# Kernel tuning notes

Hardware: AMD Instinct MI355X
Metric: run time of the kernel (lower is better)

## Reference

```python
import jax, jax.numpy as jnp
import numpy as np

NUM_CLASSES = 17
NUM_ENSEMBLE = 10
TAU = 10.0
TOP_K = 20  # min(self.k=20, filter_K=200)
EPS = 1e-12


def _l2norm(x, axis=-1):
    # matches F.normalize: x / max(||x||, 1e-12)
    n = jnp.sqrt(jnp.sum(x * x, axis=axis, keepdims=True))
    return x / jnp.maximum(n, EPS)


def _batch_ensemble(x, weight, alpha_be, gamma_be, ensemble_bias):
    # x: [M, D1] -> [E, M, D2]  (BatchEnsemble.forward, kept in [E, M, D2] layout)
    r = x[None, :, :] * alpha_be[:, None, :]              # [E, M, D1]
    w = jnp.einsum('emd,od->emo', r, weight)              # [E, M, D2]
    return w * gamma_be[:, None, :] + ensemble_bias[:, None, :]


def _compute_logits(z, supports, labels, weight, alpha_be, gamma_be, ensemble_bias):
    mlp_z = _batch_ensemble(z, weight, alpha_be, gamma_be, ensemble_bias)         # [E, B, D2]
    mlp_s = _batch_ensemble(supports, weight, alpha_be, gamma_be, ensemble_bias)  # [E, N, D2]
    lbl = labels / (jnp.sum(labels, axis=0, keepdims=True) + EPS)                 # [N, C]
    centroids = jnp.einsum('nc,end->ecd', lbl, mlp_s)                             # [E, C, D2]
    zn = _l2norm(mlp_z)
    cn = _l2norm(centroids)
    return TAU * jnp.einsum('ebd,ecd->ebc', zn, cn)                               # [E, B, C]


def _cosine_distance(X, Y):
    Xn = _l2norm(X, axis=1)
    Yn = _l2norm(Y, axis=1)
    XX = jnp.sum(Xn * Xn, axis=1)[:, None]   # [B, 1]
    YY = jnp.sum(Yn * Yn, axis=1)            # [N]
    XY = 2.0 * (Xn @ Yn.T)                   # [B, N]
    return XX + YY - XY


def _target_generation(z, supports, labels, weight, alpha_be, gamma_be, ensemble_bias):
    dist = _cosine_distance(z, supports)      # [B, N]
    W = jnp.exp(-dist)
    B = W.shape[0]
    _, idx = jax.lax.top_k(W, TOP_K)                                   # [B, K]
    mask = jnp.zeros_like(W).at[jnp.arange(B)[:, None], idx].set(1.0)  # [B, N]
    temp = _compute_logits(supports, supports, labels, weight, alpha_be, gamma_be, ensemble_bias)  # [E, N, C]
    tgt_oh = jax.nn.one_hot(jnp.argmax(temp, axis=-1), NUM_CLASSES, dtype=temp.dtype)  # [E, N, C]
    soft = jax.nn.softmax(temp, axis=-1)
    targets = jnp.einsum('bn,enc->ebc', mask, tgt_oh)
    targets = targets / (jnp.sum(targets, axis=2, keepdims=True) + EPS)
    outputs = jnp.einsum('bn,enc->ebc', mask, soft)
    outputs = outputs / (jnp.sum(outputs, axis=2, keepdims=True) + EPS)
    outputs = jnp.mean(outputs, axis=0)   # [B, C]
    return targets, outputs


def setup_inputs() -> dict:
    key = jax.random.key(0)
    ks = jax.random.split(key, 7)
    B, N, D1, D2, E, C = 4096, 3400, 2048, 1024, NUM_ENSEMBLE, NUM_CLASSES
    z = jax.random.normal(ks[0], (B, D1), dtype=jnp.float32)
    supports = jax.random.normal(ks[1], (N, D1), dtype=jnp.float32)
    y = jax.random.randint(ks[2], (N,), 0, C)
    labels = jax.nn.one_hot(y, C, dtype=jnp.float32)
    weight = jax.random.normal(ks[3], (D2, D1), dtype=jnp.float32) * 0.02
    alpha_be = 1.0 + 0.1 * jax.random.normal(ks[4], (E, D1), dtype=jnp.float32)
    gamma_be = 1.0 + 0.1 * jax.random.normal(ks[5], (E, D2), dtype=jnp.float32)
    ensemble_bias = jnp.zeros((E, D2), dtype=jnp.float32)
    return {"z": z, "supports": supports, "labels": labels, "weight": weight,
            "alpha_be": alpha_be, "gamma_be": gamma_be, "ensemble_bias": ensemble_bias}


def reference(z, supports, labels, weight, alpha_be, gamma_be, ensemble_bias):
    targets, outputs = _target_generation(z, supports, labels, weight, alpha_be, gamma_be, ensemble_bias)
    logits = _compute_logits(z, supports, labels, weight, alpha_be, gamma_be, ensemble_bias)  # [E, B, C]
    return outputs, logits
```

## Files before the change

kernel.cpp:

```cpp
#include <hip/hip_runtime.h>
#include <math.h>

#define B_    4096
#define N_    3400
#define NP2_  3584
#define D1_   2048
#define D2_   1024
#define E_    10
#define NE_   (E_ * D2_)
#define NDOT_ 256
#define NEX_  (NE_ + NDOT_)
#define ZOFF_ 3456
#define MR_   7680
#define EC_   170
#define C_    17
#define TOPK_ 20
#define CAND_ 24
#define TAU_  10.0f

typedef __bf16 bf16x8 __attribute__((ext_vector_type(8)));
typedef __bf16 bf16x4 __attribute__((ext_vector_type(4)));
typedef float  f32x4  __attribute__((ext_vector_type(4)));

#define MFMA_(a,b,c) __builtin_amdgcn_mfma_f32_16x16x32_bf16(a,b,c,0,0,0)

__device__ inline float wsum64(float v){
  #pragma unroll
  for (int m = 1; m < 64; m <<= 1) v += __shfl_xor(v, m);
  return v;
}

__device__ __forceinline__ void gload_lds16(const unsigned short* g, unsigned short* l){
  __builtin_amdgcn_global_load_lds(
      (const __attribute__((address_space(1))) void*)g,
      (__attribute__((address_space(3))) void*)l, 16, 0, 0);
}

__global__ __launch_bounds__(256)
void prep_rows(const float* __restrict__ X, unsigned short* __restrict__ hi,
               float* __restrict__ rinv){
  const int r = blockIdx.x, t = threadIdx.x;
  const float4* x4 = reinterpret_cast<const float4*>(X + (long)r * D1_);
  bf16x4* h4 = reinterpret_cast<bf16x4*>(hi + (long)r * D1_);
  float ss = 0.f;
  #pragma unroll
  for (int it = 0; it < 2; ++it){
    int i = t + it * 256;
    float4 v = x4[i];
    float f[4] = {v.x, v.y, v.z, v.w};
    bf16x4 h;
    #pragma unroll
    for (int j = 0; j < 4; ++j){
      ss += f[j] * f[j];
      h[j] = (__bf16)f[j];
    }
    h4[i] = h;
  }
  __shared__ float red[256];
  red[t] = ss; __syncthreads();
  for (int s = 128; s; s >>= 1){ if (t < s) red[t] += red[t + s]; __syncthreads(); }
  if (t == 0) rinv[r] = 1.f / fmaxf(sqrtf(red[0]), 1e-12f);
}

__global__ __launch_bounds__(256)
void zfill_all(uint4* p0, long n0, uint4* p1, long n1, uint4* p2, long n2,
               uint4* p3, long n3, uint4* p4, long n4){
  long i = (long)blockIdx.x * 256 + threadIdx.x;
  uint4 zz = make_uint4(0,0,0,0);
  if (i < n0){ p0[i] = zz; return; } i -= n0;
  if (i < n1){ p1[i] = zz; return; } i -= n1;
  if (i < n2){ p2[i] = zz; return; } i -= n2;
  if (i < n3){ p3[i] = zz; return; } i -= n3;
  if (i < n4){ p4[i] = zz; }
}

__global__ __launch_bounds__(256)
void labelprep(const float* __restrict__ labels, int* __restrict__ y, float* __restrict__ cnt){
  int n = blockIdx.x * 256 + threadIdx.x;
  if (n >= N_) return;
  int c = 0;
  #pragma unroll
  for (int cc = 0; cc < C_; ++cc) if (labels[n * C_ + cc] > 0.5f) c = cc;
  y[n] = c;
  atomicAdd(&cnt[c], 1.0f);
}

__global__ __launch_bounds__(256)
void wfold(const float* __restrict__ W, const float* __restrict__ alpha,
           unsigned short* __restrict__ wbf){
  long i = (long)blockIdx.x * 256 + threadIdx.x;
  const long perE = (long)D2_ * D1_ / 4;
  int e = (int)(i / perE);
  long r = i - (long)e * perE;
  int k4 = (int)(r & (D1_/4 - 1));
  float4 wv = reinterpret_cast<const float4*>(W)[r];
  float4 av = reinterpret_cast<const float4*>(alpha + (long)e * D1_)[k4];
  bf16x4 o;
  o[0] = (__bf16)(wv.x * av.x);
  o[1] = (__bf16)(wv.y * av.y);
  o[2] = (__bf16)(wv.z * av.z);
  o[3] = (__bf16)(wv.w * av.w);
  reinterpret_cast<bf16x4*>(wbf)[i] = o;
}

__global__ __launch_bounds__(256)
void transposeW(const float* __restrict__ W, float* __restrict__ WT){
  __shared__ float tile[32][33];
  const int bx = blockIdx.x, by = blockIdx.y;
  const int tx = threadIdx.x & 31, ty = threadIdx.x >> 5;
  #pragma unroll
  for (int i = 0; i < 4; ++i)
    tile[ty + i*8][tx] = W[(long)(by*32 + ty + i*8) * D1_ + bx*32 + tx];
  __syncthreads();
  #pragma unroll
  for (int i = 0; i < 4; ++i)
    WT[(long)(bx*32 + ty + i*8) * D2_ + by*32 + tx] = tile[tx][ty + i*8];
}

__global__ __launch_bounds__(256)
void pbuild(const float* __restrict__ S, const int* __restrict__ y,
            const float* __restrict__ cnt, float* __restrict__ part){
  __shared__ float acc[C_ * 256];
  __shared__ float winv[C_];
  const int t = threadIdx.x, kb = blockIdx.x * 256, s = blockIdx.y;
  #pragma unroll
  for (int c = 0; c < C_; ++c) acc[c * 256 + t] = 0.f;
  if (t < C_) winv[t] = 1.f / (cnt[t] + 1e-12f);
  __syncthreads();
  const int n0 = s * 425, n1 = n0 + 425;
  for (int n = n0; n < n1; ++n){
    int c = y[n];
    acc[c * 256 + t] += winv[c] * S[(long)n * D1_ + kb + t];
  }
  #pragma unroll
  for (int c = 0; c < C_; ++c)
    part[((long)s * C_ + c) * D1_ + kb + t] = acc[c * 256 + t];
}

__global__ __launch_bounds__(256)
void pa2(const float* __restrict__ part, const float* __restrict__ alpha,
         float* __restrict__ A2){
  int i = blockIdx.x * 256 + threadIdx.x;
  if (i >= EC_ * D1_) return;
  int ec = i >> 11, k = i & (D1_ - 1);
  int e = ec / C_, c = ec - e * C_;
  float s = 0.f;
  #pragma unroll
  for (int kz = 0; kz < 8; ++kz) s += part[((long)kz * C_ + c) * D1_ + k];
  A2[i] = s * alpha[(long)e * D1_ + k];
}

__global__ __launch_bounds__(256)
void redcent(const float* __restrict__ part2, const float* __restrict__ gamma,
             const float* __restrict__ bias, const float* __restrict__ cnt,
             float* __restrict__ cent){
  int i = blockIdx.x * 256 + threadIdx.x;
  if (i >= EC_ * D2_) return;
  int ec = i >> 10, d = i & (D2_ - 1);
  int e = ec / C_, c = ec - e * C_;
  float s = 0.f;
  #pragma unroll
  for (int kz = 0; kz < 8; ++kz) s += part2[(long)kz * EC_ * D2_ + i];
  float sc = cnt[c] / (cnt[c] + 1e-12f);
  cent[i] = gamma[(long)e * D2_ + d] * s + bias[(long)e * D2_ + d] * sc;
}

__global__ __launch_bounds__(256)
void normgcn(float* __restrict__ cent, const float* __restrict__ gamma,
             const float* __restrict__ bias, float* __restrict__ gcn,
             float* __restrict__ bconst){
  const int ec = blockIdx.x, t = threadIdx.x;
  const int e = ec / C_;
  float4* c4 = reinterpret_cast<float4*>(cent + (long)ec * D2_);
  float4 v = c4[t];
  float ss = v.x*v.x + v.y*v.y + v.z*v.z + v.w*v.w;
  __shared__ float red[256];
  red[t] = ss; __syncthreads();
  for (int s = 128; s; s >>= 1){ if (t < s) red[t] += red[t + s]; __syncthreads(); }
  float rinv = 1.f / fmaxf(sqrtf(red[0]), 1e-12f);
  v.x *= rinv; v.y *= rinv; v.z *= rinv; v.w *= rinv;
  c4[t] = v;
  float4 g = reinterpret_cast<const float4*>(gamma + (long)e * D2_)[t];
  reinterpret_cast<float4*>(gcn + (long)ec * D2_)[t] =
      make_float4(g.x*v.x, g.y*v.y, g.z*v.z, g.w*v.w);
  float4 bb = reinterpret_cast<const float4*>(bias + (long)e * D2_)[t];
  float bs = bb.x*v.x + bb.y*v.y + bb.z*v.z + bb.w*v.w;
  __syncthreads();
  red[t] = bs; __syncthreads();
  for (int s = 128; s; s >>= 1){ if (t < s) red[t] += red[t + s]; __syncthreads(); }
  if (t == 0) bconst[ec] = red[0];
}

__global__ __launch_bounds__(256)
void redgb(const float* __restrict__ part2, const float* __restrict__ alpha,
           unsigned short* __restrict__ wbf){
  int i = blockIdx.x * 256 + threadIdx.x;
  if (i >= EC_ * D1_) return;
  int ec = i >> 11, k = i & (D1_ - 1);
  int e = ec / C_;
  float s = 0.f;
  #pragma unroll
  for (int kz = 0; kz < 8; ++kz) s += part2[(long)kz * EC_ * D1_ + i];
  __bf16 b = (__bf16)(alpha[(long)e * D1_ + k] * s);
  wbf[(long)(NE_ + ec) * D1_ + k] = *(unsigned short*)&b;
}

__global__ __launch_bounds__(256)
void gemm64k(const float* __restrict__ A, int lda,
             const float* __restrict__ Bm, int ldb,
             float* __restrict__ part, int M, int N, int KC)
{
  __shared__ float As[16][68];
  __shared__ float Bs[16][68];
  const int kz = blockIdx.z;
  const int m0 = blockIdx.y * 64, n0 = blockIdx.x * 64;
  const int t  = threadIdx.x;
  const int lr = t >> 2;
  const int lk = (t & 3) << 2;
  const int ty4 = (t >> 4) << 2;
  const int tx4 = (t & 15) << 2;
  const bool aok = (m0 + lr) < M;
  const bool bok = (n0 + lr) < N;
  const float* ap = A  + (long)(m0 + lr) * lda + lk;
  const float* bp = Bm + (long)(n0 + lr) * ldb + lk;
  float acc[4][4] = {{0.f}};
  const int k0b = kz * KC, k0e = k0b + KC;
  for (int k0 = k0b; k0 < k0e; k0 += 16){
    float4 av = make_float4(0,0,0,0), bv = make_float4(0,0,0,0);
    if (aok) av = *reinterpret_cast<const float4*>(ap + k0);
    if (bok) bv = *reinterpret_cast<const float4*>(bp + k0);
    As[lk+0][lr] = av.x; As[lk+1][lr] = av.y; As[lk+2][lr] = av.z; As[lk+3][lr] = av.w;
    Bs[lk+0][lr] = bv.x; Bs[lk+1][lr] = bv.y; Bs[lk+2][lr] = bv.z; Bs[lk+3][lr] = bv.w;
    __syncthreads();
    #pragma unroll
    for (int kk = 0; kk < 16; ++kk){
      float4 a = *reinterpret_cast<const float4*>(&As[kk][ty4]);
      float4 b = *reinterpret_cast<const float4*>(&Bs[kk][tx4]);
      float aa[4] = {a.x, a.y, a.z, a.w};
      float bb[4] = {b.x, b.y, b.z, b.w};
      #pragma unroll
      for (int i = 0; i < 4; ++i)
        #pragma unroll
        for (int j = 0; j < 4; ++j)
          acc[i][j] += aa[i] * bb[j];
    }
    __syncthreads();
  }
  float* Out = part + (long)kz * M * N;
  #pragma unroll
  for (int i = 0; i < 4; ++i){
    int m = m0 + ty4 + i;
    if (m >= M) continue;
    #pragma unroll
    for (int j = 0; j < 4; ++j){
      int n = n0 + tx4 + j;
      if (n >= N) continue;
      Out[(long)m * N + n] = acc[i][j];
    }
  }
}

__global__ __launch_bounds__(512)
void sc2(const unsigned short* __restrict__ zh, const unsigned short* __restrict__ sh,
         const float* __restrict__ zinv, const float* __restrict__ sinv,
         float* __restrict__ Out)
{
  __shared__ unsigned short LA[2][16384];
  __shared__ unsigned short LB[2][16384];
  const int n0 = blockIdx.x * 256;
  const int m0 = blockIdx.y * 256;
  const int t = threadIdx.x, lane = t & 63, w = t >> 6;
  const int wm = w >> 2, wn = w & 3;
  const int r15 = lane & 15, kb = lane >> 4;

  const unsigned short* a0p = zh + (long)(m0 +       w*16 + r15) * D1_ + kb*8;
  const unsigned short* a1p = zh + (long)(m0 + 128 + w*16 + r15) * D1_ + kb*8;
  const unsigned short* b0p = sh + (long)(n0 +       w*16 + r15) * D1_ + kb*8;
  const unsigned short* b1p = sh + (long)(n0 + 128 + w*16 + r15) * D1_ + kb*8;
  const unsigned d00 = (unsigned)(w*2)*512,     d01 = (unsigned)(w*2+1)*512;
  const unsigned d10 = (unsigned)((8+w)*2)*512, d11 = (unsigned)((8+w)*2+1)*512;
  const unsigned raB = (unsigned)wm*8192 + (unsigned)lane*8;
  const unsigned rbB = (unsigned)wn*4096 + (unsigned)lane*8;

#define STAGE_SC(buf, kt) do{ const int ko = (kt)*64; \
    gload_lds16(a0p+ko,    &LA[buf][d00]); gload_lds16(a0p+ko+32, &LA[buf][d01]); \
    gload_lds16(a1p+ko,    &LA[buf][d10]); gload_lds16(a1p+ko+32, &LA[buf][d11]); \
    gload_lds16(b0p+ko,    &LB[buf][d00]); gload_lds16(b0p+ko+32, &LB[buf][d01]); \
    gload_lds16(b1p+ko,    &LB[buf][d10]); gload_lds16(b1p+ko+32, &LB[buf][d11]); }while(0)

  f32x4 acc[8][4];
  #pragma unroll
  for (int i = 0; i < 8; ++i)
    #pragma unroll
    for (int j = 0; j < 4; ++j)
      acc[i][j] = (f32x4){0.f, 0.f, 0.f, 0.f};

  STAGE_SC(0, 0);
  asm volatile("s_waitcnt vmcnt(0)" ::: "memory");
  __builtin_amdgcn_sched_barrier(0);
  __builtin_amdgcn_s_barrier();

  for (int kt = 0; kt < 32; ++kt){
    const int cb = kt & 1;
    if (kt < 31) STAGE_SC(cb ^ 1, kt + 1);

    bf16x8 ar[4][2], br[4][2];
    #pragma unroll
    for (int i = 0; i < 4; ++i){
      ar[i][0] = *(const bf16x8*)&LA[cb][raB + (unsigned)(i*2  )*512];
      ar[i][1] = *(const bf16x8*)&LA[cb][raB + (unsigned)(i*2+1)*512];
    }
    #pragma unroll
    for (int j = 0; j < 4; ++j){
      br[j][0] = *(const bf16x8*)&LB[cb][rbB + (unsigned)(j*2  )*512];
      br[j][1] = *(const bf16x8*)&LB[cb][rbB + (unsigned)(j*2+1)*512];
    }
    asm volatile("s_waitcnt lgkmcnt(0)" ::: "memory");
    __builtin_amdgcn_sched_barrier(0);
    __builtin_amdgcn_s_setprio(1);
    #pragma unroll
    for (int ks = 0; ks < 2; ++ks)
      #pragma unroll
      for (int i = 0; i < 4; ++i)
        #pragma unroll
        for (int j = 0; j < 4; ++j)
          acc[i][j] = MFMA_(ar[i][ks], br[j][ks], acc[i][j]);
    __builtin_amdgcn_s_setprio(0);
    #pragma unroll
    for (int i = 0; i < 4; ++i){
      ar[i][0] = *(const bf16x8*)&LA[cb][raB + (unsigned)((4+i)*2  )*512];
      ar[i][1] = *(const bf16x8*)&LA[cb][raB + (unsigned)((4+i)*2+1)*512];
    }
    asm volatile("s_waitcnt lgkmcnt(0)" ::: "memory");
    __builtin_amdgcn_sched_barrier(0);
    __builtin_amdgcn_s_setprio(1);
    #pragma unroll
    for (int ks = 0; ks < 2; ++ks)
      #pragma unroll
      for (int i = 0; i < 4; ++i)
        #pragma unroll
        for (int j = 0; j < 4; ++j)
          acc[4+i][j] = MFMA_(ar[i][ks], br[j][ks], acc[4+i][j]);
    __builtin_amdgcn_s_setprio(0);

    asm volatile("s_waitcnt vmcnt(0)" ::: "memory");
    __builtin_amdgcn_sched_barrier(0);
    __builtin_amdgcn_s_barrier();
  }
#undef STAGE_SC

  const int mb = m0 + wm * 128 + kb * 4;
  const int nc0 = n0 + wn * 64 + r15;
  #pragma unroll
  for (int j = 0; j < 4; ++j){
    int n = nc0 + j * 16;
    if (n >= N_) continue;
    float si = sinv[n];
    #pragma unroll
    for (int i = 0; i < 8; ++i)
      #pragma unroll
      for (int r = 0; r < 4; ++r){
        int m = mb + i*16 + r;
        Out[(long)m * N_ + n] = acc[i][j][r] * zinv[m] * si;
      }
  }
}

__global__ __launch_bounds__(512)
void nd2(const unsigned short* __restrict__ A,
         const unsigned short* __restrict__ Bw,
         const float* __restrict__ gamma,
         const float* __restrict__ bias,
         float* __restrict__ norm2,
         float* __restrict__ dots)
{
  __shared__ unsigned short LA[2][16384];
  __shared__ unsigned short LB[2][16384];
  const int n0 = blockIdx.x * 256;
  const int m0 = blockIdx.y * 256;
  const int t = threadIdx.x, lane = t & 63, w = t >> 6;
  const int wm = w >> 2, wn = w & 3;
  const int r15 = lane & 15, kb = lane >> 4;

  const unsigned short* a0p = A  + (long)(m0 +       w*16 + r15) * D1_ + kb*8;
  const unsigned short* a1p = A  + (long)(m0 + 128 + w*16 + r15) * D1_ + kb*8;
  const unsigned short* b0p = Bw + (long)(n0 +       w*16 + r15) * D1_ + kb*8;
  const unsigned short* b1p = Bw + (long)(n0 + 128 + w*16 + r15) * D1_ + kb*8;
  const unsigned d00 = (unsigned)(w*2)*512,     d01 = (unsigned)(w*2+1)*512;
  const unsigned d10 = (unsigned)((8+w)*2)*512, d11 = (unsigned)((8+w)*2+1)*512;
  const unsigned raB = (unsigned)wm*8192 + (unsigned)lane*8;
  const unsigned rbB = (unsigned)wn*4096 + (unsigned)lane*8;

#define STAGE_ND(buf, kt) do{ const int ko = (kt)*64; \
    gload_lds16(a0p+ko,    &LA[buf][d00]); gload_lds16(a0p+ko+32, &LA[buf][d01]); \
    gload_lds16(a1p+ko,    &LA[buf][d10]); gload_lds16(a1p+ko+32, &LA[buf][d11]); \
    gload_lds16(b0p+ko,    &LB[buf][d00]); gload_lds16(b0p+ko+32, &LB[buf][d01]); \
    gload_lds16(b1p+ko,    &LB[buf][d10]); gload_lds16(b1p+ko+32, &LB[buf][d11]); }while(0)

  f32x4 acc[8][4];
  #pragma unroll
  for (int i = 0; i < 8; ++i)
    #pragma unroll
    for (int j = 0; j < 4; ++j)
      acc[i][j] = (f32x4){0.f, 0.f, 0.f, 0.f};

  STAGE_ND(0, 0);
  asm volatile("s_waitcnt vmcnt(0)" ::: "memory");
  __builtin_amdgcn_sched_barrier(0);
  __builtin_amdgcn_s_barrier();

  for (int kt = 0; kt < 32; ++kt){
    const int cb = kt & 1;
    if (kt < 31) STAGE_ND(cb ^ 1, kt + 1);

    bf16x8 ar[4][2], br[4][2];
    #pragma unroll
    for (int i = 0; i < 4; ++i){
      ar[i][0] = *(const bf16x8*)&LA[cb][raB + (unsigned)(i*2  )*512];
      ar[i][1] = *(const bf16x8*)&LA[cb][raB + (unsigned)(i*2+1)*512];
    }
    #pragma unroll
    for (int j = 0; j < 4; ++j){
      br[j][0] = *(const bf16x8*)&LB[cb][rbB + (unsigned)(j*2  )*512];
      br[j][1] = *(const bf16x8*)&LB[cb][rbB + (unsigned)(j*2+1)*512];
    }
    asm volatile("s_waitcnt lgkmcnt(0)" ::: "memory");
    __builtin_amdgcn_sched_barrier(0);
    __builtin_amdgcn_s_setprio(1);
    #pragma unroll
    for (int ks = 0; ks < 2; ++ks)
      #pragma unroll
      for (int i = 0; i < 4; ++i)
        #pragma unroll
        for (int j = 0; j < 4; ++j)
          acc[i][j] = MFMA_(ar[i][ks], br[j][ks], acc[i][j]);
    __builtin_amdgcn_s_setprio(0);
    #pragma unroll
    for (int i = 0; i < 4; ++i){
      ar[i][0] = *(const bf16x8*)&LA[cb][raB + (unsigned)((4+i)*2  )*512];
      ar[i][1] = *(const bf16x8*)&LA[cb][raB + (unsigned)((4+i)*2+1)*512];
    }
    asm volatile("s_waitcnt lgkmcnt(0)" ::: "memory");
    __builtin_amdgcn_sched_barrier(0);
    __builtin_amdgcn_s_setprio(1);
    #pragma unroll
    for (int ks = 0; ks < 2; ++ks)
      #pragma unroll
      for (int i = 0; i < 4; ++i)
        #pragma unroll
        for (int j = 0; j < 4; ++j)
          acc[4+i][j] = MFMA_(ar[i][ks], br[j][ks], acc[4+i][j]);
    __builtin_amdgcn_s_setprio(0);

    asm volatile("s_waitcnt vmcnt(0)" ::: "memory");
    __builtin_amdgcn_sched_barrier(0);
    __builtin_amdgcn_s_barrier();
  }
#undef STAGE_ND

  if (n0 < NE_){
    const int e = n0 >> 10;
    float g4[4], b4[4];
    #pragma unroll
    for (int j = 0; j < 4; ++j){
      int n = n0 + wn * 64 + j * 16 + r15;
      g4[j] = gamma[n]; b4[j] = bias[n];
    }
    float rs[32];
    #pragma unroll
    for (int i = 0; i < 8; ++i)
      #pragma unroll
      for (int r = 0; r < 4; ++r){
        float s = 0.f;
        #pragma unroll
        for (int j = 0; j < 4; ++j){
          float v = acc[i][j][r] * g4[j] + b4[j];
          s += v * v;
        }
        rs[i*4 + r] = s;
      }
    #pragma unroll
    for (int msk = 1; msk < 16; msk <<= 1)
      #pragma unroll
      for (int q = 0; q < 32; ++q) rs[q] += __shfl_xor(rs[q], msk);
    float* red = (float*)&LA[0][0];
    if (r15 == 0){
      #pragma unroll
      for (int i = 0; i < 8; ++i)
        #pragma unroll
        for (int r = 0; r < 4; ++r)
          red[w * 128 + i*16 + kb*4 + r] = rs[i*4 + r];
    }
    __syncthreads();
    if (t < 256){
      int wmg = t >> 7;
      float v = 0.f;
      #pragma unroll
      for (int q = 0; q < 4; ++q)
        v += red[(wmg*4 + q) * 128 + (t & 127)];
      atomicAdd(&norm2[(long)(m0 + t) * E_ + e], v);
    }
  } else {
    const int dc0 = n0 - NE_ + wn * 64 + r15;
    const int mb = m0 + wm * 128 + kb * 4;
    #pragma unroll
    for (int j = 0; j < 4; ++j){
      int dc = dc0 + j * 16;
      #pragma unroll
      for (int i = 0; i < 8; ++i)
        #pragma unroll
        for (int r = 0; r < 4; ++r)
          dots[(long)(mb + i*16 + r) * NDOT_ + dc] = acc[i][j][r];
    }
  }
}

__global__ __launch_bounds__(256)
void topk_rescore(const float* __restrict__ scores, const float* __restrict__ z,
                  const float* __restrict__ S, const float* __restrict__ sinv,
                  int* __restrict__ idx){
  const int b = blockIdx.x, t = threadIdx.x;
  const int l = t & 63, wid = t >> 6;
  const float* row = scores + (long)b * N_;
  float v[14];
  #pragma unroll
  for (int j = 0; j < 14; ++j){
    int i = t + j * 256;
    v[j] = (i < N_) ? row[i] : -3.0e38f;
  }
  __shared__ float wv4[4];
  __shared__ int   wi4[4];
  __shared__ int   cand[CAND_];
  __shared__ float sval[CAND_];
  for (int it = 0; it < CAND_; ++it){
    float bv = -3.0e38f; int bj = 0;
    #pragma unroll
    for (int j = 0; j < 14; ++j)
      if (v[j] > bv){ bv = v[j]; bj = j; }
    int bi = t + bj * 256;
    #pragma unroll
    for (int m = 1; m < 64; m <<= 1){
      float ov = __shfl_xor(bv, m);
      int   oi = __shfl_xor(bi, m);
      if (ov > bv || (ov == bv && oi < bi)){ bv = ov; bi = oi; }
    }
    if (l == 0){ wv4[wid] = bv; wi4[wid] = bi; }
    __syncthreads();
    float gv = wv4[0]; int gi = wi4[0];
    #pragma unroll
    for (int k = 1; k < 4; ++k){
      float ov = wv4[k]; int oi = wi4[k];
      if (ov > gv || (ov == gv && oi < gi)){ gv = ov; gi = oi; }
    }
    if (t == 0) cand[it] = gi;
    const int ot = gi & 255, oj = gi >> 8;
    #pragma unroll
    for (int j = 0; j < 14; ++j)
      if (t == ot && j == oj) v[j] = -3.0e38f;
    __syncthreads();
  }
  const float4* zr = reinterpret_cast<const float4*>(z + (long)b * D1_);
  for (int ci = wid; ci < CAND_; ci += 4){
    int n = cand[ci];
    const float4* sr = reinterpret_cast<const float4*>(S + (long)n * D1_);
    float p = 0.f;
    #pragma unroll
    for (int j = 0; j < 8; ++j){
      float4 a = zr[l + j * 64];
      float4 c = sr[l + j * 64];
      p += a.x*c.x + a.y*c.y + a.z*c.z + a.w*c.w;
    }
    p = wsum64(p);
    if (l == 0) sval[ci] = p * sinv[n];
  }
  __syncthreads();
  if (t < 64){
    float vv = (l < CAND_) ? sval[l] : -3.0e38f;
    int   nn = (l < CAND_) ? cand[l] : 0x7fffffff;
    for (int it = 0; it < TOPK_; ++it){
      float bv = vv; int bi = nn, bl = l;
      #pragma unroll
      for (int m = 1; m < 64; m <<= 1){
        float ov = __shfl_xor(bv, m);
        int   oi = __shfl_xor(bi, m);
        int   ol = __shfl_xor(bl, m);
        if (ov > bv || (ov == bv && oi < bi)){ bv = ov; bi = oi; bl = ol; }
      }
      if (l == 0) idx[b * TOPK_ + it] = bi;
      if (l == bl) vv = -3.0e38f;
    }
  }
}

__global__ __launch_bounds__(256)
void soft_build(const float* __restrict__ dots, const float* __restrict__ norm2,
                const float* __restrict__ bconst, float* __restrict__ soft){
  int id = blockIdx.x * 256 + threadIdx.x;
  if (id >= N_ * E_) return;
  int e = id % E_, n = id / E_;
  float rinv = 1.f / fmaxf(sqrtf(norm2[(long)n * E_ + e]), 1e-12f);
  float tv[C_];
  #pragma unroll
  for (int c = 0; c < C_; ++c)
    tv[c] = TAU_ * (dots[(long)n * NDOT_ + e*C_ + c] + bconst[e*C_ + c]) * rinv;
  float m = tv[0];
  #pragma unroll
  for (int c = 1; c < C_; ++c) m = fmaxf(m, tv[c]);
  float p[C_]; float sum = 0.f;
  #pragma unroll
  for (int c = 0; c < C_; ++c){ p[c] = expf(tv[c] - m); sum += p[c]; }
  float is = 1.f / sum;
  #pragma unroll
  for (int c = 0; c < C_; ++c)
    soft[((long)e * N_ + n) * C_ + c] = p[c] * is;
}

__global__ __launch_bounds__(256)
void logits_fin(const float* __restrict__ dots, const float* __restrict__ norm2,
                const float* __restrict__ bconst, float* __restrict__ out){
  int id = blockIdx.x * 256 + threadIdx.x;
  if (id >= B_ * E_) return;
  int e = id % E_, b = id / E_;
  int m = ZOFF_ + b;
  float rinv = 1.f / fmaxf(sqrtf(norm2[(long)m * E_ + e]), 1e-12f);
  float* op = out + (size_t)B_ * C_ + ((long)e * B_ + b) * C_;
  #pragma unroll
  for (int c = 0; c < C_; ++c)
    op[c] = TAU_ * (dots[(long)m * NDOT_ + e*C_ + c] + bconst[e*C_ + c]) * rinv;
}

__global__ __launch_bounds__(256)
void outputs_k(const float* __restrict__ soft, const int* __restrict__ idx, float* __restrict__ out){
  const int lane = threadIdx.x & 63;
  const int b = blockIdx.x * 4 + (threadIdx.x >> 6);
  const int* id = idx + b * TOPK_;
  float o = 0.f;
  for (int e = 0; e < E_; ++e){
    float S = 0.f;
    const float* se = soft + (long)e * N_ * C_;
    #pragma unroll
    for (int k = 0; k < TOPK_; ++k){
      int n = id[k];
      if (lane < C_) S += se[(long)n * C_ + lane];
    }
    float tot = wsum64(S);
    o += S / (tot + 1e-12f);
  }
  if (lane < C_) out[(long)b * C_ + lane] = o * (1.f / E_);
}

extern "C" void kernel_launch(void* const* d_in, const int* in_sizes, int n_in,
                              void* d_out, int out_size, void* d_ws, size_t ws_size,
                              hipStream_t stream){
  const float* z        = (const float*)d_in[0];
  const float* supports = (const float*)d_in[1];
  const float* labels   = (const float*)d_in[2];
  const float* weight   = (const float*)d_in[3];
  const float* alpha    = (const float*)d_in[4];
  const float* gamma    = (const float*)d_in[5];
  const float* bias     = (const float*)d_in[6];
  float* out = (float*)d_out;

  char* w = (char*)d_ws;
  size_t off = 0;
  auto alloc = [&](size_t bytes)->char*{
    char* p = w + off;
    off = (off + bytes + 255) & ~(size_t)255;
    return p;
  };

  float* zinv = (float*)alloc((size_t)B_ * 4);
  float* sinv = (float*)alloc((size_t)N_ * 4);
  float* cnt  = (float*)alloc((size_t)C_ * 4);
  int*   y    = (int*)  alloc((size_t)N_ * 4);
  int*   idx  = (int*)  alloc((size_t)B_ * TOPK_ * 4);
  unsigned short* SZ  = (unsigned short*)alloc((size_t)MR_ * D1_ * 2);
  unsigned short* wbf = (unsigned short*)alloc((size_t)NEX_ * D1_ * 2);
  float* WT     = (float*)alloc((size_t)D1_ * D2_ * 4);
  float* part   = (float*)alloc((size_t)8 * C_ * D1_ * 4);
  float* A2     = (float*)alloc((size_t)EC_ * D1_ * 4);
  float* cent   = (float*)alloc((size_t)EC_ * D2_ * 4);
  float* gcn    = (float*)alloc((size_t)EC_ * D2_ * 4);
  float* bconst = (float*)alloc((size_t)256 * 4);
  float* scores = (float*)alloc((size_t)B_ * N_ * 4);
  float* dots   = (float*)alloc((size_t)MR_ * NDOT_ * 4);
  float* norm2  = (float*)alloc((size_t)MR_ * E_ * 4);
  float* soft   = (float*)alloc((size_t)E_ * N_ * C_ * 4);
  float* part2  = (float*)alloc((size_t)8 * EC_ * D1_ * 4);
  (void)ws_size; (void)in_sizes; (void)n_in; (void)out_size;

  unsigned short* sh = SZ;
  unsigned short* zh = SZ + (size_t)ZOFF_ * D1_;

  {
    long n0 = 14336, n1 = 32768, n2 = 22016, n3 = 19200, n4 = 5;
    long tot = n0 + n1 + n2 + n3 + n4;
    zfill_all<<<(int)((tot + 255) / 256), 256, 0, stream>>>(
        (uint4*)(sh + (size_t)N_ * D1_), n0,
        (uint4*)(SZ + (size_t)(ZOFF_ + B_) * D1_), n1,
        (uint4*)(wbf + (size_t)(NE_ + EC_) * D1_), n2,
        (uint4*)norm2, n3,
        (uint4*)cnt, n4);
  }
  labelprep<<<(N_ + 255) / 256, 256, 0, stream>>>(labels, y, cnt);

  prep_rows<<<B_, 256, 0, stream>>>(z, zh, zinv);
  prep_rows<<<N_, 256, 0, stream>>>(supports, sh, sinv);
  wfold<<<(int)((long)NE_ * D1_ / 4 / 256), 256, 0, stream>>>(weight, alpha, wbf);
  transposeW<<<dim3(D1_ / 32, D2_ / 32), 256, 0, stream>>>(weight, WT);

  sc2<<<dim3(NP2_ / 256, B_ / 256, 1), 512, 0, stream>>>(
      zh, sh, zinv, sinv, scores);
  topk_rescore<<<B_, 256, 0, stream>>>(scores, z, supports, sinv, idx);

  pbuild<<<dim3(D1_ / 256, 8), 256, 0, stream>>>(supports, y, cnt, part);
  pa2<<<(EC_ * D1_ + 255) / 256, 256, 0, stream>>>(part, alpha, A2);
  gemm64k<<<dim3(D2_ / 64, 3, 8), 256, 0, stream>>>(
      A2, D1_, weight, D1_, part2, EC_, D2_, 256);
  redcent<<<(EC_ * D2_ + 255) / 256, 256, 0, stream>>>(part2, gamma, bias, cnt, cent);
  normgcn<<<EC_, 256, 0, stream>>>(cent, gamma, bias, gcn, bconst);
  gemm64k<<<dim3(D1_ / 64, 3, 8), 256, 0, stream>>>(
      gcn, D2_, WT, D2_, part2, EC_, D1_, 128);
  redgb<<<(EC_ * D1_ + 255) / 256, 256, 0, stream>>>(part2, alpha, wbf);

  nd2<<<dim3(NEX_ / 256, MR_ / 256, 1), 512, 0, stream>>>(
      SZ, wbf, gamma, bias, norm2, dots);

  soft_build<<<(N_ * E_ + 255) / 256, 256, 0, stream>>>(dots, norm2, bconst, soft);
  outputs_k<<<B_ / 4, 256, 0, stream>>>(soft, idx, out);
  logits_fin<<<(B_ * E_ + 255) / 256, 256, 0, stream>>>(dots, norm2, bconst, out);
}
```

Measured before the change: 1.003 ms.

## Restructure bf16 GEMM main loops into 8-phase ping-pong schedule with split loads

Both 256x256 MFMA GEMM kernels (sc2 and the batch-ensemble GEMM) replace the simple double-buffered loop with an 8-phase schedule per two K-tiles. Each phase issues a quarter of the next tile's global-to-LDS loads, reads one quarter of the operands from LDS, and runs a quarter of the MFMAs. Barriers and a partial vmcnt wait replace the full drain at the end of every tile. The aim is to spread memory traffic evenly across the compute so it overlaps better, at the cost of many more workgroup barriers and tighter buffer-reuse ordering that must stay race-free.

Measured after the change: 897.9 us, median of 2. -10.5%, faster.

```diff
diff --git a/kernel.cpp b/kernel.cpp
--- a/kernel.cpp
+++ b/kernel.cpp
@@ -260,6 +260,93 @@
   }
 }
 
+#define SA0(buf, kt) { gload_lds16(a0p+(kt)*64, &LA[buf][d00]); gload_lds16(a0p+(kt)*64+32, &LA[buf][d01]); }
+#define SA1(buf, kt) { gload_lds16(a1p+(kt)*64, &LA[buf][d10]); gload_lds16(a1p+(kt)*64+32, &LA[buf][d11]); }
+#define SB0(buf, kt) { gload_lds16(b0p+(kt)*64, &LB[buf][d00]); gload_lds16(b0p+(kt)*64+32, &LB[buf][d01]); }
+#define SB1(buf, kt) { gload_lds16(b1p+(kt)*64, &LB[buf][d10]); gload_lds16(b1p+(kt)*64+32, &LB[buf][d11]); }
+
+#define RD_A03(cb) { _Pragma("unroll") for (int i = 0; i < 4; ++i){ \
+    ar[i][0] = *(const bf16x8*)&LA[cb][raB + (unsigned)(i*2  )*512]; \
+    ar[i][1] = *(const bf16x8*)&LA[cb][raB + (unsigned)(i*2+1)*512]; } }
+#define RD_A47(cb) { _Pragma("unroll") for (int i = 0; i < 4; ++i){ \
+    ar[i][0] = *(const bf16x8*)&LA[cb][raB + (unsigned)((4+i)*2  )*512]; \
+    ar[i][1] = *(const bf16x8*)&LA[cb][raB + (unsigned)((4+i)*2+1)*512]; } }
+#define RD_B01(cb) { _Pragma("unroll") for (int j = 0; j < 2; ++j){ \
+    brA[j][0] = *(const bf16x8*)&LB[cb][rbB + (unsigned)(j*2  )*512]; \
+    brA[j][1] = *(const bf16x8*)&LB[cb][rbB + (unsigned)(j*2+1)*512]; } }
+#define RD_B23(cb) { _Pragma("unroll") for (int j = 0; j < 2; ++j){ \
+    brB[j][0] = *(const bf16x8*)&LB[cb][rbB + (unsigned)((2+j)*2  )*512]; \
+    brB[j][1] = *(const bf16x8*)&LB[cb][rbB + (unsigned)((2+j)*2+1)*512]; } }
+
+#define MM_Q0 { _Pragma("unroll") for (int ks = 0; ks < 2; ++ks) \
+    _Pragma("unroll") for (int i = 0; i < 4; ++i) \
+    _Pragma("unroll") for (int j = 0; j < 2; ++j) \
+      acc[i][j] = MFMA_(ar[i][ks], brA[j][ks], acc[i][j]); }
+#define MM_Q1 { _Pragma("unroll") for (int ks = 0; ks < 2; ++ks) \
+    _Pragma("unroll") for (int i = 0; i < 4; ++i) \
+    _Pragma("unroll") for (int j = 0; j < 2; ++j) \
+      acc[i][2+j] = MFMA_(ar[i][ks], brB[j][ks], acc[i][2+j]); }
+#define MM_Q2 { _Pragma("unroll") for (int ks = 0; ks < 2; ++ks) \
+    _Pragma("unroll") for (int i = 0; i < 4; ++i) \
+    _Pragma("unroll") for (int j = 0; j < 2; ++j) \
+      acc[4+i][2+j] = MFMA_(ar[i][ks], brB[j][ks], acc[4+i][2+j]); }
+#define MM_Q3 { _Pragma("unroll") for (int ks = 0; ks < 2; ++ks) \
+    _Pragma("unroll") for (int i = 0; i < 4; ++i) \
+    _Pragma("unroll") for (int j = 0; j < 2; ++j) \
+      acc[4+i][j] = MFMA_(ar[i][ks], brA[j][ks], acc[4+i][j]); }
+
+#define PH_TAIL \
+  __builtin_amdgcn_s_barrier(); \
+  asm volatile("s_waitcnt lgkmcnt(0)" ::: "memory"); \
+  __builtin_amdgcn_sched_barrier(0); \
+  __builtin_amdgcn_s_setprio(1);
+#define PH_END \
+  __builtin_amdgcn_s_setprio(0); \
+  __builtin_amdgcn_s_barrier();
+#define PH_END_W(more) \
+  __builtin_amdgcn_s_setprio(0); \
+  if (more) asm volatile("s_waitcnt vmcnt(4)" ::: "memory"); \
+  else      asm volatile("s_waitcnt vmcnt(0)" ::: "memory"); \
+  __builtin_amdgcn_sched_barrier(0); \
+  __builtin_amdgcn_s_barrier();
+
+#define K8_LOOP \
+  bf16x8 ar[4][2], brA[2][2], brB[2][2]; \
+   \
+  SA0(0, 0); SA1(0, 0); SB0(0, 0); SB1(0, 0); \
+  SB0(1, 1); SB1(1, 1); \
+  asm volatile("s_waitcnt vmcnt(4)" ::: "memory"); \
+  __builtin_amdgcn_sched_barrier(0); \
+  __builtin_amdgcn_s_barrier(); \
+  for (int it = 0; it < 16; ++it){ \
+    const int kt = it * 2; \
+    const bool more = (it < 15); \
+     \
+    RD_A03(0); RD_B01(0); SA0(1, kt + 1); \
+    PH_TAIL; MM_Q0; PH_END; \
+     \
+    RD_B23(0); SA1(1, kt + 1); \
+    PH_TAIL; MM_Q1; PH_END; \
+     \
+    RD_A47(0); if (more) SB0(0, kt + 2); \
+    PH_TAIL; MM_Q2; PH_END; \
+     \
+    if (more) SB1(0, kt + 2); \
+    PH_TAIL; MM_Q3; PH_END_W(more); \
+     \
+    RD_A03(1); RD_B01(1); if (more) SA0(0, kt + 2); \
+    PH_TAIL; MM_Q0; PH_END; \
+     \
+    RD_B23(1); if (more) SA1(0, kt + 2); \
+    PH_TAIL; MM_Q1; PH_END; \
+     \
+    RD_A47(1); if (more) SB0(1, kt + 3); \
+    PH_TAIL; MM_Q2; PH_END; \
+     \
+    if (more) SB1(1, kt + 3); \
+    PH_TAIL; MM_Q3; PH_END_W(more); \
+  }
+
 __global__ __launch_bounds__(512)
 void sc2(const unsigned short* __restrict__ zh, const unsigned short* __restrict__ sh,
          const float* __restrict__ zinv, const float* __restrict__ sinv,
@@ -282,12 +369,6 @@
   const unsigned raB = (unsigned)wm*8192 + (unsigned)lane*8;
   const unsigned rbB = (unsigned)wn*4096 + (unsigned)lane*8;
 
-#define STAGE_SC(buf, kt) do{ const int ko = (kt)*64; \
-    gload_lds16(a0p+ko,    &LA[buf][d00]); gload_lds16(a0p+ko+32, &LA[buf][d01]); \
-    gload_lds16(a1p+ko,    &LA[buf][d10]); gload_lds16(a1p+ko+32, &LA[buf][d11]); \
-    gload_lds16(b0p+ko,    &LB[buf][d00]); gload_lds16(b0p+ko+32, &LB[buf][d01]); \
-    gload_lds16(b1p+ko,    &LB[buf][d10]); gload_lds16(b1p+ko+32, &LB[buf][d11]); }while(0)
-
   f32x4 acc[8][4];
   #pragma unroll
   for (int i = 0; i < 8; ++i)
@@ -295,59 +376,7 @@
     for (int j = 0; j < 4; ++j)
       acc[i][j] = (f32x4){0.f, 0.f, 0.f, 0.f};
 
-  STAGE_SC(0, 0);
-  asm volatile("s_waitcnt vmcnt(0)" ::: "memory");
-  __builtin_amdgcn_sched_barrier(0);
-  __builtin_amdgcn_s_barrier();
-
-  for (int kt = 0; kt < 32; ++kt){
-    const int cb = kt & 1;
-    if (kt < 31) STAGE_SC(cb ^ 1, kt + 1);
-
-    bf16x8 ar[4][2], br[4][2];
-    #pragma unroll
-    for (int i = 0; i < 4; ++i){
-      ar[i][0] = *(const bf16x8*)&LA[cb][raB + (unsigned)(i*2  )*512];
-      ar[i][1] = *(const bf16x8*)&LA[cb][raB + (unsigned)(i*2+1)*512];
-    }
-    #pragma unroll
-    for (int j = 0; j < 4; ++j){
-      br[j][0] = *(const bf16x8*)&LB[cb][rbB + (unsigned)(j*2  )*512];
-      br[j][1] = *(const bf16x8*)&LB[cb][rbB + (unsigned)(j*2+1)*512];
-    }
-    asm volatile("s_waitcnt lgkmcnt(0)" ::: "memory");
-    __builtin_amdgcn_sched_barrier(0);
-    __builtin_amdgcn_s_setprio(1);
-    #pragma unroll
-    for (int ks = 0; ks < 2; ++ks)
-      #pragma unroll
-      for (int i = 0; i < 4; ++i)
-        #pragma unroll
-        for (int j = 0; j < 4; ++j)
-          acc[i][j] = MFMA_(ar[i][ks], br[j][ks], acc[i][j]);
-    __builtin_amdgcn_s_setprio(0);
-    #pragma unroll
-    for (int i = 0; i < 4; ++i){
-      ar[i][0] = *(const bf16x8*)&LA[cb][raB + (unsigned)((4+i)*2  )*512];
-      ar[i][1] = *(const bf16x8*)&LA[cb][raB + (unsigned)((4+i)*2+1)*512];
-    }
-    asm volatile("s_waitcnt lgkmcnt(0)" ::: "memory");
-    __builtin_amdgcn_sched_barrier(0);
-    __builtin_amdgcn_s_setprio(1);
-    #pragma unroll
-    for (int ks = 0; ks < 2; ++ks)
-      #pragma unroll
-      for (int i = 0; i < 4; ++i)
-        #pragma unroll
-        for (int j = 0; j < 4; ++j)
-          acc[4+i][j] = MFMA_(ar[i][ks], br[j][ks], acc[4+i][j]);
-    __builtin_amdgcn_s_setprio(0);
-
-    asm volatile("s_waitcnt vmcnt(0)" ::: "memory");
-    __builtin_amdgcn_sched_barrier(0);
-    __builtin_amdgcn_s_barrier();
-  }
-#undef STAGE_SC
+  K8_LOOP
 
   const int mb = m0 + wm * 128 + kb * 4;
   const int nc0 = n0 + wn * 64 + r15;
@@ -391,12 +420,6 @@
   const unsigned raB = (unsigned)wm*8192 + (unsigned)lane*8;
   const unsigned rbB = (unsigned)wn*4096 + (unsigned)lane*8;
 
-#define STAGE_ND(buf, kt) do{ const int ko = (kt)*64; \
-    gload_lds16(a0p+ko,    &LA[buf][d00]); gload_lds16(a0p+ko+32, &LA[buf][d01]); \
-    gload_lds16(a1p+ko,    &LA[buf][d10]); gload_lds16(a1p+ko+32, &LA[buf][d11]); \
-    gload_lds16(b0p+ko,    &LB[buf][d00]); gload_lds16(b0p+ko+32, &LB[buf][d01]); \
-    gload_lds16(b1p+ko,    &LB[buf][d10]); gload_lds16(b1p+ko+32, &LB[buf][d11]); }while(0)
-
   f32x4 acc[8][4];
   #pragma unroll
   for (int i = 0; i < 8; ++i)
@@ -404,59 +427,7 @@
     for (int j = 0; j < 4; ++j)
       acc[i][j] = (f32x4){0.f, 0.f, 0.f, 0.f};
 
-  STAGE_ND(0, 0);
-  asm volatile("s_waitcnt vmcnt(0)" ::: "memory");
-  __builtin_amdgcn_sched_barrier(0);
-  __builtin_amdgcn_s_barrier();
-
-  for (int kt = 0; kt < 32; ++kt){
-    const int cb = kt & 1;
-    if (kt < 31) STAGE_ND(cb ^ 1, kt + 1);
-
-    bf16x8 ar[4][2], br[4][2];
-    #pragma unroll
-    for (int i = 0; i < 4; ++i){
-      ar[i][0] = *(const bf16x8*)&LA[cb][raB + (unsigned)(i*2  )*512];
-      ar[i][1] = *(const bf16x8*)&LA[cb][raB + (unsigned)(i*2+1)*512];
-    }
-    #pragma unroll
-    for (int j = 0; j < 4; ++j){
-      br[j][0] = *(const bf16x8*)&LB[cb][rbB + (unsigned)(j*2  )*512];
-      br[j][1] = *(const bf16x8*)&LB[cb][rbB + (unsigned)(j*2+1)*512];
-    }
-    asm volatile("s_waitcnt lgkmcnt(0)" ::: "memory");
-    __builtin_amdgcn_sched_barrier(0);
-    __builtin_amdgcn_s_setprio(1);
-    #pragma unroll
-    for (int ks = 0; ks < 2; ++ks)
-      #pragma unroll
-      for (int i = 0; i < 4; ++i)
-        #pragma unroll
-        for (int j = 0; j < 4; ++j)
-          acc[i][j] = MFMA_(ar[i][ks], br[j][ks], acc[i][j]);
-    __builtin_amdgcn_s_setprio(0);
-    #pragma unroll
-    for (int i = 0; i < 4; ++i){
-      ar[i][0] = *(const bf16x8*)&LA[cb][raB + (unsigned)((4+i)*2  )*512];
-      ar[i][1] = *(const bf16x8*)&LA[cb][raB + (unsigned)((4+i)*2+1)*512];
-    }
-    asm volatile("s_waitcnt lgkmcnt(0)" ::: "memory");
-    __builtin_amdgcn_sched_barrier(0);
-    __builtin_amdgcn_s_setprio(1);
-    #pragma unroll
-    for (int ks = 0; ks < 2; ++ks)
-      #pragma unroll
-      for (int i = 0; i < 4; ++i)
-        #pragma unroll
-        for (int j = 0; j < 4; ++j)
-          acc[4+i][j] = MFMA_(ar[i][ks], br[j][ks], acc[4+i][j]);
-    __builtin_amdgcn_s_setprio(0);
-
-    asm volatile("s_waitcnt vmcnt(0)" ::: "memory");
-    __builtin_amdgcn_sched_barrier(0);
-    __builtin_amdgcn_s_barrier();
-  }
-#undef STAGE_ND
+  K8_LOOP
 
   if (n0 < NE_){
     const int e = n0 >> 10;
```
